# Kernel tuning notes

Hardware: AMD Instinct MI355X
Metric: run time of the kernel (lower is better)

## Reference

```python
import jax, jax.numpy as jnp
import numpy as np

NUM_HEADS = 8
GROUPS = 32
EPS = 1e-5


def group_norm(x, gamma, beta):
    # x: [b, c, l]; normalize over (c//GROUPS, l) per group
    b, c, l = x.shape
    xg = x.reshape(b, GROUPS, -1)
    mu = jnp.mean(xg, axis=-1, keepdims=True)
    var = jnp.mean(jnp.square(xg - mu), axis=-1, keepdims=True)
    xn = ((xg - mu) * jax.lax.rsqrt(var + EPS)).reshape(b, c, l)
    return xn * gamma[None, :, None] + beta[None, :, None]


def setup_inputs() -> dict:
    key = jax.random.key(0)
    ks = jax.random.split(key, 8)
    b, c, h, w = 8, 512, 64, 64
    cc, cl = 768, 256
    inner = 512
    s = lambda fan_in: 1.0 / np.sqrt(fan_in)
    return {
        "x": jax.random.normal(ks[0], (b, c, h, w), jnp.float32),
        "context": jax.random.normal(ks[1], (b, cc, cl), jnp.float32),
        "gnx_g": jnp.ones((c,), jnp.float32),
        "gnx_b": jnp.zeros((c,), jnp.float32),
        "gnc_g": jnp.ones((cc,), jnp.float32),
        "gnc_b": jnp.zeros((cc,), jnp.float32),
        "wq": jax.random.normal(ks[2], (inner, c), jnp.float32) * s(c),
        "bq": jax.random.normal(ks[3], (inner,), jnp.float32) * s(c),
        "wkv": jax.random.normal(ks[4], (2 * inner, cc), jnp.float32) * s(cc),
        "bkv": jax.random.normal(ks[5], (2 * inner,), jnp.float32) * s(cc),
        "wo": jax.random.normal(ks[6], (c, inner), jnp.float32) * s(inner),
        "bo": jax.random.normal(ks[7], (c,), jnp.float32) * s(inner),
    }


def reference(x, context, gnx_g, gnx_b, gnc_g, gnc_b, wq, bq, wkv, bkv, wo, bo):
    b, c, h, w = x.shape
    xf = x.reshape(b, c, h * w)                      # [b, c, L]
    inner = wq.shape[0]
    dh = inner // NUM_HEADS
    scale = dh ** (-0.5)

    q = jnp.einsum('oc,bcl->bol', wq, group_norm(xf, gnx_g, gnx_b)) + bq[None, :, None]
    kv = jnp.einsum('oc,bcl->bol', wkv, group_norm(context, gnc_g, gnc_b)) + bkv[None, :, None]
    k, v = jnp.split(kv, 2, axis=1)                  # [b, inner, S] each

    L = xf.shape[-1]
    S = k.shape[-1]
    q = q.reshape(b * NUM_HEADS, dh, L)
    k = k.reshape(b * NUM_HEADS, dh, S)
    v = v.reshape(b * NUM_HEADS, dh, S)

    # Faithful double-scale quirk: effective scaling is 1/dh
    dots = jnp.einsum('bct,bcs->bts', q * scale, k * scale)   # [bH, L, S]
    attn = jax.nn.softmax(dots.astype(jnp.float32), axis=-1).astype(dots.dtype)
    out = jnp.einsum('bts,bcs->bct', attn, v)                 # [bH, dh, L]
    out = out.reshape(b, inner, L)
    out = jnp.einsum('oc,bcl->bol', wo, out) + bo[None, :, None]
    return (xf + out).reshape(b, c, h, w)
```

## Files before the change

kernel.cpp:

```cpp
#include <hip/hip_runtime.h>

typedef unsigned short u16;
typedef unsigned int u32;
typedef __bf16 bf16x8 __attribute__((ext_vector_type(8)));
typedef float f32x4 __attribute__((ext_vector_type(4)));

__device__ __forceinline__ u16 f2bf(float f) {
    return __builtin_bit_cast(u16, (__bf16)f);
}
__device__ __forceinline__ u32 pkbf(float a, float b) {
    return (u32)__builtin_bit_cast(u16, (__bf16)a) |
           ((u32)__builtin_bit_cast(u16, (__bf16)b) << 16);
}
__device__ __forceinline__ u32 pku(u16 a, u16 b) {
    return (u32)a | ((u32)b << 16);
}
__device__ __forceinline__ bf16x8 ldb8(const void* p) {
    return __builtin_bit_cast(bf16x8, *(const uint4*)p);
}
__device__ __forceinline__ f32x4 mfma16(bf16x8 a, bf16x8 b, f32x4 c) {
    return __builtin_amdgcn_mfma_f32_16x16x32_bf16(a, b, c, 0, 0, 0);
}

__global__ __launch_bounds__(256) void cvt_w(const float* __restrict__ in,
                                             u16* __restrict__ out, int n4) {
    int i = blockIdx.x * 256 + threadIdx.x;
    const int stride = gridDim.x * 256;
    for (; i < n4; i += stride) {
        float4 v = ((const float4*)in)[i];
        ((uint2*)out)[i] = make_uint2(pkbf(v.x, v.y), pkbf(v.z, v.w));
    }
}

__global__ __launch_bounds__(256) void gn_stats(const float* __restrict__ in,
                                                float2* __restrict__ stats, int N) {
    const int tid = threadIdx.x;
    const long base = (long)blockIdx.x * N;
    float s = 0.f, s2 = 0.f;
    for (int i = tid * 4; i < N; i += 256 * 4) {
        float4 v = *(const float4*)(in + base + i);
        s += v.x + v.y + v.z + v.w;
        s2 += v.x * v.x + v.y * v.y + v.z * v.z + v.w * v.w;
    }
#pragma unroll
    for (int m = 1; m < 64; m <<= 1) { s += __shfl_xor(s, m); s2 += __shfl_xor(s2, m); }
    __shared__ float ps[4], ps2[4];
    const int w = tid >> 6;
    if ((tid & 63) == 0) { ps[w] = s; ps2[w] = s2; }
    __syncthreads();
    if (tid == 0) {
        float S = ps[0] + ps[1] + ps[2] + ps[3];
        float S2 = ps2[0] + ps2[1] + ps2[2] + ps2[3];
        float mu = S / (float)N;
        float var = S2 / (float)N - mu * mu;
        stats[blockIdx.x] = make_float2(mu, rsqrtf(var + 1e-5f));
    }
}


__global__ __launch_bounds__(256) void gn_tr(const float* __restrict__ ctx,
                                             const float2* __restrict__ stats,
                                             const float* __restrict__ gamma,
                                             const float* __restrict__ beta,
                                             u16* __restrict__ ctx_t) {
    __shared__ u16 T[64][64];
    const int tid = threadIdx.x;
    const int b = blockIdx.z;
    const int c0 = blockIdx.x * 64, s0 = blockIdx.y * 64;
#pragma unroll
    for (int r = 0; r < 4; ++r) {
        int idx = r * 256 + tid;
        int c = idx >> 4, s4 = (idx & 15) << 2;
        int cg = c0 + c;
        float4 v = *(const float4*)(ctx + ((long)b * 768 + cg) * 256 + s0 + s4);
        float2 st = stats[b * 32 + cg / 24];
        float gm = gamma[cg], bt = beta[cg];
        float vv[4] = {(v.x - st.x) * st.y * gm + bt, (v.y - st.x) * st.y * gm + bt,
                       (v.z - st.x) * st.y * gm + bt, (v.w - st.x) * st.y * gm + bt};
#pragma unroll
        for (int jj = 0; jj < 4; ++jj) {
            int j = (jj + (tid & 3)) & 3;
            int row = s4 + j;
            T[row][c ^ ((row & 7) << 3)] = f2bf(vv[j]);
        }
    }
    __syncthreads();
#pragma unroll
    for (int r = 0; r < 2; ++r) {
        int f = r * 256 + tid;
        int s = f >> 3, cf = (f & 7) << 3;
        uint4 vv = *(const uint4*)&T[s][cf ^ ((s & 7) << 3)];
        *(uint4*)(ctx_t + ((long)b * 256 + s0 + s) * 768 + c0 + cf) = vv;
    }
}

__global__ __launch_bounds__(256, 2) void gemm_kv2(
    const u16* __restrict__ W, const u16* __restrict__ ctx_t,
    const float* __restrict__ bias, u16* __restrict__ k_t, u16* __restrict__ vout) {
    constexpr int K = 768;
    const int tid = threadIdx.x;
    const int b = blockIdx.z;
    const int o0 = blockIdx.x * 64;
    const int s0 = blockIdx.y * 64;
    const int lane = tid & 63, wv = tid >> 6;
    const int l16 = lane & 15, g = lane >> 4;

    const u16* ap = W + (long)(o0 + wv * 16 + l16) * K;
    const u16* ct = ctx_t + ((long)b * 256 + s0) * K;

    f32x4 acc[4] = {};
#pragma unroll
    for (int kc = 0; kc < 24; ++kc) {
        const int k8 = kc * 32 + g * 8;
        bf16x8 afr = ldb8(ap + k8);
#pragma unroll
        for (int ni = 0; ni < 4; ++ni) {
            bf16x8 bfr = ldb8(ct + (long)(ni * 16 + l16) * K + k8);
            acc[ni] = mfma16(afr, bfr, acc[ni]);
        }
    }
    const int orow = o0 + wv * 16 + g * 4;
    if (blockIdx.x < 8) {
        const int h = blockIdx.x;
        const int d0 = wv * 16 + g * 4;
        const float b0 = bias[orow], b1 = bias[orow + 1];
        const float b2 = bias[orow + 2], b3 = bias[orow + 3];
#pragma unroll
        for (int ni = 0; ni < 4; ++ni) {
            int s = s0 + ni * 16 + l16;
            *(uint2*)(k_t + (((long)b * 8 + h) * 256 + s) * 64 + d0) =
                make_uint2(pkbf(acc[ni][0] + b0, acc[ni][1] + b1),
                           pkbf(acc[ni][2] + b2, acc[ni][3] + b3));
        }
    } else {
#pragma unroll
        for (int ni = 0; ni < 4; ++ni) {
            int s = s0 + ni * 16 + l16;
#pragma unroll
            for (int i = 0; i < 4; ++i) {
                int vr = orow - 512 + i;
                vout[((long)b * 512 + vr) * 256 + s] = f2bf(acc[ni][i] + bias[orow + i]);
            }
        }
    }
}

template <int MODE>
__global__ __launch_bounds__(256, 2) void big_gemm(
    const u16* __restrict__ W, const void* __restrict__ Bsrc,
    const float2* __restrict__ stats, const float* __restrict__ gamma,
    const float* __restrict__ beta, const float* __restrict__ bias,
    const float* __restrict__ X, void* __restrict__ outp) {
    constexpr int K = 512, N = 4096, CPG = 16;
    __shared__ u16 Blds[64][64];
    const int tid = threadIdx.x;
    const int b = blockIdx.z;
    const int n0 = blockIdx.x * 64;
    const int lane = tid & 63, w = tid >> 6;
    const int l16 = lane & 15, g = lane >> 4;

    f32x4 acc[8][4] = {};
    for (int c = 0; c < 8; ++c) {
        const int k0 = c * 64;
        __syncthreads();
        if (MODE == 0) {
            const float* Bb = (const float*)Bsrc + (long)b * K * N;
#pragma unroll
            for (int r = 0; r < 4; ++r) {
                int idx = r * 256 + tid;
                int kk = idx >> 4;
                int n4 = (idx & 15) << 2;
                int kg = k0 + kk;
                float4 v = *(const float4*)(Bb + (long)kg * N + n0 + n4);
                float2 st = stats[b * 32 + kg / CPG];
                float gm = gamma[kg], bt = beta[kg];
                v.x = (v.x - st.x) * st.y * gm + bt;
                v.y = (v.y - st.x) * st.y * gm + bt;
                v.z = (v.z - st.x) * st.y * gm + bt;
                v.w = (v.w - st.x) * st.y * gm + bt;
                float vv[4] = {v.x, v.y, v.z, v.w};
#pragma unroll
                for (int jj = 0; jj < 4; ++jj) {
                    int j = (jj + (lane & 3)) & 3;
                    int row = n4 + j;
                    Blds[row][kk ^ ((row & 7) << 3)] = f2bf(vv[j]);
                }
            }
        } else {
            const u16* Ob = (const u16*)Bsrc + (((long)b * 8 + c) * 4096 + n0) * 64;
#pragma unroll
            for (int r = 0; r < 2; ++r) {
                int idx = r * 256 + tid;
                int t = idx >> 3;
                int d0 = (idx & 7) << 3;
                uint4 vv = *(const uint4*)(Ob + (long)t * 64 + d0);
                *(uint4*)&Blds[t][d0 ^ ((t & 7) << 3)] = vv;
            }
        }
        __syncthreads();
#pragma unroll
        for (int kk = 0; kk < 2; ++kk) {
            bf16x8 bfr[4];
#pragma unroll
            for (int ni = 0; ni < 4; ++ni) {
                int row = ni * 16 + l16;
                bfr[ni] = ldb8(&Blds[row][(kk * 32 + g * 8) ^ ((row & 7) << 3)]);
            }
#pragma unroll
            for (int mi = 0; mi < 8; ++mi) {
                int arow = w * 128 + mi * 16 + l16;
                bf16x8 afr = ldb8(W + (long)arow * K + k0 + kk * 32 + g * 8);
#pragma unroll
                for (int ni = 0; ni < 4; ++ni)
                    acc[mi][ni] = mfma16(afr, bfr[ni], acc[mi][ni]);
            }
        }
    }
    if (MODE == 0) {
        u16* qt = (u16*)outp;
#pragma unroll
        for (int mi = 0; mi < 8; ++mi) {
            int h = w * 2 + (mi >> 2);
            int dbase = (mi & 3) * 16 + g * 4;
#pragma unroll
            for (int ni = 0; ni < 4; ++ni) {
                int col = n0 + ni * 16 + l16;
                float v0 = acc[mi][ni][0] + bias[h * 64 + dbase + 0];
                float v1 = acc[mi][ni][1] + bias[h * 64 + dbase + 1];
                float v2 = acc[mi][ni][2] + bias[h * 64 + dbase + 2];
                float v3 = acc[mi][ni][3] + bias[h * 64 + dbase + 3];
                *(uint2*)(qt + (((long)b * 8 + h) * 4096 + col) * 64 + dbase) =
                    make_uint2(pkbf(v0, v1), pkbf(v2, v3));
            }
        }
    } else {
        float* out = (float*)outp;
        const long ob = (long)b * K * N;
#pragma unroll
        for (int mi = 0; mi < 8; ++mi)
#pragma unroll
            for (int i = 0; i < 4; ++i) {
                int row = w * 128 + mi * 16 + g * 4 + i;
                float bs = bias[row];
#pragma unroll
                for (int ni = 0; ni < 4; ++ni) {
                    int col = n0 + ni * 16 + l16;
                    long off = ob + (long)row * N + col;
                    out[off] = acc[mi][ni][i] + bs + X[off];
                }
            }
    }
}

__global__ __launch_bounds__(256, 1) void attn_v9(const u16* __restrict__ qt_in,
                                                  const u16* __restrict__ k_t,
                                                  const u16* __restrict__ v,
                                                  u16* __restrict__ qt_out) {
    __shared__ u16 kT[256][64];
    __shared__ u16 Vp[64][256];
    const int tid = threadIdx.x;
    const int bh = blockIdx.y;
    const int b = bh >> 3, h = bh & 7;
    const int lane = tid & 63, w = tid >> 6;
    const int l16 = lane & 15, g = lane >> 4;

    const long kb = (long)bh * 256 * 64;
    const long vb = ((long)(b * 512 + h * 64)) * 256;
    const long qb = (long)bh * 4096 * 64 + (long)blockIdx.x * 512 * 64;

#pragma unroll
    for (int r = 0; r < 8; ++r) {
        int idx = r * 256 + tid;
        int s = idx >> 3, d0 = (idx & 7) << 3;
        uint4 vv = *(const uint4*)(k_t + kb + (long)s * 64 + d0);
        *(uint4*)&kT[s][d0 ^ ((s & 7) << 3)] = vv;
    }
#pragma unroll
    for (int r = 0; r < 8; ++r) {
        int idx = r * 256 + tid;
        int d = idx >> 5, s0 = (idx & 31) << 3;
        union { uint4 v4; u16 h8[8]; } u;
        u.v4 = *(const uint4*)(v + vb + (long)d * 256 + s0);
        int f = s0 >> 4, g2 = (s0 >> 2) & 3;
        int cl = ((f >> 1) << 5) + (g2 << 3) + ((f & 1) << 2);
        int sw = (d & 7) << 3;
        *(uint2*)&Vp[d][cl ^ sw] = make_uint2(pku(u.h8[0], u.h8[1]), pku(u.h8[2], u.h8[3]));
        *(uint2*)&Vp[d][(cl + 8) ^ sw] = make_uint2(pku(u.h8[4], u.h8[5]), pku(u.h8[6], u.h8[7]));
    }
    __syncthreads();

    const float aa = 0.015625f * 1.44269504f;
    bf16x8 bq0, bq1;
    {
        const u16* qp = qt_in + qb + (long)(w * 16 + l16) * 64;
        bq0 = ldb8(qp + g * 8);
        bq1 = ldb8(qp + 32 + g * 8);
    }
    for (int it = 0; it < 8; ++it) {
        const int tcol = it * 64 + w * 16 + l16;
        f32x4 sacc[16] = {};
#pragma unroll
        for (int mc = 0; mc < 4; ++mc) {
#pragma unroll
            for (int kk = 0; kk < 2; ++kk) {
                bf16x8 bqk = kk ? bq1 : bq0;
#pragma unroll
                for (int j = 0; j < 4; ++j) {
                    int mi = mc * 4 + j;
                    bf16x8 ak = ldb8(&kT[mi * 16 + l16][(kk * 32 + g * 8) ^ ((l16 & 7) << 3)]);
                    sacc[mi] = mfma16(ak, bqk, sacc[mi]);
                }
            }
        }
        if (it < 7) {
            const u16* qp = qt_in + qb + (long)(tcol + 64) * 64;
            bq0 = ldb8(qp + g * 8);
            bq1 = ldb8(qp + 32 + g * 8);
        }
        float s0 = 0.f, s1 = 0.f, s2 = 0.f, s3 = 0.f;
#pragma unroll
        for (int f = 0; f < 16; ++f) {
            float p0 = exp2f(sacc[f][0] * aa);
            float p1 = exp2f(sacc[f][1] * aa);
            float p2 = exp2f(sacc[f][2] * aa);
            float p3 = exp2f(sacc[f][3] * aa);
            sacc[f][0] = p0; sacc[f][1] = p1; sacc[f][2] = p2; sacc[f][3] = p3;
            s0 += p0; s1 += p1; s2 += p2; s3 += p3;
        }
        float sum = (s0 + s1) + (s2 + s3);
        sum += __shfl_xor(sum, 16);
        sum += __shfl_xor(sum, 32);
        const float inv = 1.0f / sum;
        f32x4 oacc[4] = {};
#pragma unroll
        for (int ks = 0; ks < 8; ++ks) {
            bf16x8 bp = __builtin_bit_cast(bf16x8,
                make_uint4(pkbf(sacc[2 * ks][0], sacc[2 * ks][1]),
                           pkbf(sacc[2 * ks][2], sacc[2 * ks][3]),
                           pkbf(sacc[2 * ks + 1][0], sacc[2 * ks + 1][1]),
                           pkbf(sacc[2 * ks + 1][2], sacc[2 * ks + 1][3])));
#pragma unroll
            for (int mi = 0; mi < 4; ++mi) {
                bf16x8 av = ldb8(&Vp[mi * 16 + l16][(ks * 32 + g * 8) ^ ((l16 & 7) << 3)]);
                oacc[mi] = mfma16(av, bp, oacc[mi]);
            }
        }
        u16* op = qt_out + qb + (long)tcol * 64;
#pragma unroll
        for (int mi = 0; mi < 4; ++mi) {
            *(uint2*)(op + mi * 16 + g * 4) = make_uint2(
                pkbf(oacc[mi][0] * inv, oacc[mi][1] * inv),
                pkbf(oacc[mi][2] * inv, oacc[mi][3] * inv));
        }
    }
}

template <bool GN, bool RESID>
__global__ __launch_bounds__(256, 2) void big_gemm_f32(
    const u16* __restrict__ W, const float* __restrict__ B,
    const float2* __restrict__ stats, const float* __restrict__ gamma,
    const float* __restrict__ beta, const float* __restrict__ bias,
    const float* __restrict__ X, float* __restrict__ out) {
    constexpr int K = 512, N = 4096, CPG = 16;
    __shared__ u16 Blds[64][64];
    const int tid = threadIdx.x;
    const int b = blockIdx.z;
    const int n0 = blockIdx.x * 64;
    const int lane = tid & 63, w = tid >> 6;
    const int l16 = lane & 15, g = lane >> 4;
    const float* Bb = B + (long)b * K * N;

    f32x4 acc[8][4] = {};
    for (int c = 0; c < 8; ++c) {
        const int k0 = c * 64;
        __syncthreads();
#pragma unroll
        for (int r = 0; r < 4; ++r) {
            int idx = r * 256 + tid;
            int kk = idx >> 4;
            int n4 = (idx & 15) << 2;
            int kg = k0 + kk;
            float4 v = *(const float4*)(Bb + (long)kg * N + n0 + n4);
            if (GN) {
                float2 st = stats[b * 32 + kg / CPG];
                float gm = gamma[kg], bt = beta[kg];
                v.x = (v.x - st.x) * st.y * gm + bt;
                v.y = (v.y - st.x) * st.y * gm + bt;
                v.z = (v.z - st.x) * st.y * gm + bt;
                v.w = (v.w - st.x) * st.y * gm + bt;
            }
            float vv[4] = {v.x, v.y, v.z, v.w};
#pragma unroll
            for (int jj = 0; jj < 4; ++jj) {
                int j = (jj + (lane & 3)) & 3;
                int row = n4 + j;
                Blds[row][kk ^ ((row & 7) << 3)] = f2bf(vv[j]);
            }
        }
        __syncthreads();
#pragma unroll
        for (int kk = 0; kk < 2; ++kk) {
            bf16x8 bfr[4];
#pragma unroll
            for (int ni = 0; ni < 4; ++ni) {
                int row = ni * 16 + l16;
                bfr[ni] = ldb8(&Blds[row][(kk * 32 + g * 8) ^ ((row & 7) << 3)]);
            }
#pragma unroll
            for (int mi = 0; mi < 8; ++mi) {
                int arow = w * 128 + mi * 16 + l16;
                bf16x8 afr = ldb8(W + (long)arow * K + k0 + kk * 32 + g * 8);
#pragma unroll
                for (int ni = 0; ni < 4; ++ni)
                    acc[mi][ni] = mfma16(afr, bfr[ni], acc[mi][ni]);
            }
        }
    }
    const long ob = (long)b * K * N;
#pragma unroll
    for (int mi = 0; mi < 8; ++mi)
#pragma unroll
        for (int i = 0; i < 4; ++i) {
            int row = w * 128 + mi * 16 + g * 4 + i;
            float bs = bias[row];
#pragma unroll
            for (int ni = 0; ni < 4; ++ni) {
                int col = n0 + ni * 16 + l16;
                long off = ob + (long)row * N + col;
                float v = acc[mi][ni][i] + bs;
                if (RESID) v += X[off];
                out[off] = v;
            }
        }
}

__global__ __launch_bounds__(256) void gemm_kv_old(
    const u16* __restrict__ W, const float* __restrict__ act,
    const float2* __restrict__ stats, const float* __restrict__ gamma,
    const float* __restrict__ beta, const float* __restrict__ bias,
    u16* __restrict__ outp, int K, int N, int CPG, long actBS, long outBS) {
    __shared__ u16 Blds[128][40];
    const int tid = threadIdx.x;
    const int b = blockIdx.z;
    const int m0 = blockIdx.y * 128;
    const int n0 = blockIdx.x * 128;
    const int lane = tid & 63;
    const int w = tid >> 6;
    const int wr = w >> 1, wc = w & 1;
    const int l16 = lane & 15, g = lane >> 4;

    const float* actB = act + (long)b * actBS;
    f32x4 acc[4][4] = {};
    for (int s = 0; s < K / 32; ++s) {
        const int k0 = s * 32;
        __syncthreads();
#pragma unroll
        for (int r = 0; r < 4; ++r) {
            int idx = r * 256 + tid;
            int kk = idx >> 5;
            int n4 = (idx & 31) << 2;
            int kg = k0 + kk;
            float2 st = stats[b * 32 + kg / CPG];
            float gm = gamma[kg], bt = beta[kg];
            float4 v = *(const float4*)(actB + (long)kg * N + n0 + n4);
            Blds[n4 + 0][kk] = f2bf((v.x - st.x) * st.y * gm + bt);
            Blds[n4 + 1][kk] = f2bf((v.y - st.x) * st.y * gm + bt);
            Blds[n4 + 2][kk] = f2bf((v.z - st.x) * st.y * gm + bt);
            Blds[n4 + 3][kk] = f2bf((v.w - st.x) * st.y * gm + bt);
        }
        __syncthreads();
        bf16x8 bfr[4];
#pragma unroll
        for (int ni = 0; ni < 4; ++ni)
            bfr[ni] = ldb8(&Blds[wc * 64 + ni * 16 + l16][g * 8]);
#pragma unroll
        for (int mi = 0; mi < 4; ++mi) {
            int row = m0 + wr * 64 + mi * 16 + l16;
            bf16x8 afr = ldb8(W + (long)row * K + k0 + g * 8);
#pragma unroll
            for (int ni = 0; ni < 4; ++ni)
                acc[mi][ni] = mfma16(afr, bfr[ni], acc[mi][ni]);
        }
    }
#pragma unroll
    for (int mi = 0; mi < 4; ++mi)
#pragma unroll
        for (int i = 0; i < 4; ++i) {
            int row = m0 + wr * 64 + mi * 16 + g * 4 + i;
            float bs = bias[row];
#pragma unroll
            for (int ni = 0; ni < 4; ++ni) {
                int col = n0 + wc * 64 + ni * 16 + l16;
                outp[(long)b * outBS + (long)row * N + col] = f2bf(acc[mi][ni][i] + bs);
            }
        }
}

__global__ __launch_bounds__(256, 2) void attn_v4(const float* q,
                                                  const u16* __restrict__ kv,
                                                  float* out) {
    __shared__ u16 kT[256][64];
    __shared__ u16 Vp[64][256];
    const int tid = threadIdx.x;
    const int bh = blockIdx.y;
    const int b = bh >> 3, h = bh & 7;
    const int lane = tid & 63, w = tid >> 6;
    const int l16 = lane & 15, g = lane >> 4;

    const long kbase = ((long)(b * 1024 + h * 64)) * 256;
    const long vbase = ((long)(b * 1024 + 512 + h * 64)) * 256;
    const long qb = ((long)(b * 512 + h * 64)) * 4096 + blockIdx.x * 512;

#pragma unroll
    for (int r = 0; r < 8; ++r) {
        int idx = r * 256 + tid;
        int d = idx >> 5, s8 = idx & 31;
        union { uint4 v; u16 h8[8]; } u;
        u.v = *(const uint4*)(kv + kbase + (long)d * 256 + s8 * 8);
#pragma unroll
        for (int j = 0; j < 8; ++j)
            kT[s8 * 8 + j][d ^ (j << 3)] = u.h8[j];
    }
#pragma unroll
    for (int r = 0; r < 8; ++r) {
        int idx = r * 256 + tid;
        int d = idx >> 5, s0 = (idx & 31) << 3;
        union { uint4 v; u16 h8[8]; } u;
        u.v = *(const uint4*)(kv + vbase + (long)d * 256 + s0);
        int f = s0 >> 4, g2 = (s0 >> 2) & 3;
        int cl = ((f >> 1) << 5) + (g2 << 3) + ((f & 1) << 2);
        int sw = (d & 7) << 3;
        *(uint2*)&Vp[d][cl ^ sw] = make_uint2(pku(u.h8[0], u.h8[1]), pku(u.h8[2], u.h8[3]));
        *(uint2*)&Vp[d][(cl + 8) ^ sw] = make_uint2(pku(u.h8[4], u.h8[5]), pku(u.h8[6], u.h8[7]));
    }
    __syncthreads();

    const float aa = 0.015625f * 1.44269504f;
    for (int it = 0; it < 8; ++it) {
        const int tcol = it * 64 + w * 16 + l16;
        u32 bqw[2][4];
#pragma unroll
        for (int kk = 0; kk < 2; ++kk) {
            const float* qp = q + qb + tcol + (long)(kk * 32 + g * 8) * 4096;
#pragma unroll
            for (int jp = 0; jp < 4; ++jp)
                bqw[kk][jp] = pkbf(qp[(2 * jp) * 4096], qp[(2 * jp + 1) * 4096]);
        }
        f32x4 sacc[16] = {};
#pragma unroll
        for (int kk = 0; kk < 2; ++kk) {
            bf16x8 bq_ = __builtin_bit_cast(bf16x8,
                make_uint4(bqw[kk][0], bqw[kk][1], bqw[kk][2], bqw[kk][3]));
#pragma unroll
            for (int mi = 0; mi < 16; ++mi) {
                bf16x8 ak = ldb8(&kT[mi * 16 + l16][(kk * 32 + g * 8) ^ ((l16 & 7) << 3)]);
                sacc[mi] = mfma16(ak, bq_, sacc[mi]);
            }
        }
        float m = -3e38f;
#pragma unroll
        for (int f = 0; f < 16; ++f)
#pragma unroll
            for (int i = 0; i < 4; ++i) m = fmaxf(m, sacc[f][i]);
        m = fmaxf(m, __shfl_xor(m, 16));
        m = fmaxf(m, __shfl_xor(m, 32));
        float m2 = m * aa;
        float sum = 0.f;
#pragma unroll
        for (int f = 0; f < 16; ++f)
#pragma unroll
            for (int i = 0; i < 4; ++i) {
                float p = exp2f(fmaf(sacc[f][i], aa, -m2));
                sacc[f][i] = p;
                sum += p;
            }
        sum += __shfl_xor(sum, 16);
        sum += __shfl_xor(sum, 32);
        const float inv = 1.0f / sum;
        f32x4 oacc[4] = {};
#pragma unroll
        for (int ks = 0; ks < 8; ++ks) {
            bf16x8 bp = __builtin_bit_cast(bf16x8,
                make_uint4(pkbf(sacc[2 * ks][0], sacc[2 * ks][1]),
                           pkbf(sacc[2 * ks][2], sacc[2 * ks][3]),
                           pkbf(sacc[2 * ks + 1][0], sacc[2 * ks + 1][1]),
                           pkbf(sacc[2 * ks + 1][2], sacc[2 * ks + 1][3])));
#pragma unroll
            for (int mi = 0; mi < 4; ++mi) {
                bf16x8 av = ldb8(&Vp[mi * 16 + l16][(ks * 32 + g * 8) ^ ((l16 & 7) << 3)]);
                oacc[mi] = mfma16(av, bp, oacc[mi]);
            }
        }
#pragma unroll
        for (int mi = 0; mi < 4; ++mi)
#pragma unroll
            for (int i = 0; i < 4; ++i)
                out[qb + (long)(mi * 16 + g * 4 + i) * 4096 + tcol] = oacc[mi][i] * inv;
    }
}

extern "C" void kernel_launch(void* const* d_in, const int* in_sizes, int n_in,
                              void* d_out, int out_size, void* d_ws, size_t ws_size,
                              hipStream_t stream) {
    const float* x     = (const float*)d_in[0];
    const float* ctx   = (const float*)d_in[1];
    const float* gnx_g = (const float*)d_in[2];
    const float* gnx_b = (const float*)d_in[3];
    const float* gnc_g = (const float*)d_in[4];
    const float* gnc_b = (const float*)d_in[5];
    const float* wq    = (const float*)d_in[6];
    const float* bq    = (const float*)d_in[7];
    const float* wkv   = (const float*)d_in[8];
    const float* bkv   = (const float*)d_in[9];
    const float* wo    = (const float*)d_in[10];
    const float* bo    = (const float*)d_in[11];
    float* out = (float*)d_out;

    char* ws = (char*)d_ws;
    float2* stats_x = (float2*)ws;
    float2* stats_c = (float2*)(ws + 2048);
    u16* wq_bf  = (u16*)(ws + 4096);
    u16* wkv_bf = (u16*)(ws + 528384);
    u16* wo_bf  = (u16*)(ws + 2101248);

    cvt_w<<<dim3(256), dim3(256), 0, stream>>>(wq, wq_bf, 512 * 512 / 4);
    cvt_w<<<dim3(256), dim3(256), 0, stream>>>(wkv, wkv_bf, 1024 * 768 / 4);
    cvt_w<<<dim3(256), dim3(256), 0, stream>>>(wo, wo_bf, 512 * 512 / 4);
    gn_stats<<<dim3(256), dim3(256), 0, stream>>>(x, stats_x, 16 * 4096);
    gn_stats<<<dim3(256), dim3(256), 0, stream>>>(ctx, stats_c, 24 * 256);

    const size_t NEED = 40374272;
    if (ws_size >= NEED) {
        u16* k_t   = (u16*)(ws + 2625536);
        u16* v     = (u16*)(ws + 4722688);
        u16* q_t   = (u16*)(ws + 6819840);
        u16* ctx_t = (u16*)(ws + 6819840);

        gn_tr<<<dim3(12, 4, 8), dim3(256), 0, stream>>>(
            ctx, stats_c, gnc_g, gnc_b, ctx_t);
        gemm_kv2<<<dim3(16, 4, 8), dim3(256), 0, stream>>>(
            wkv_bf, ctx_t, bkv, k_t, v);
        big_gemm<0><<<dim3(64, 1, 8), dim3(256), 0, stream>>>(
            wq_bf, x, stats_x, gnx_g, gnx_b, bq, nullptr, q_t);
        attn_v9<<<dim3(8, 64), dim3(256), 0, stream>>>(q_t, k_t, v, q_t);
        big_gemm<1><<<dim3(64, 1, 8), dim3(256), 0, stream>>>(
            wo_bf, q_t, nullptr, nullptr, nullptr, bo, x, out);
    } else {
        u16* kv = (u16*)(ws + 2625536);
        big_gemm_f32<true, false><<<dim3(64, 1, 8), dim3(256), 0, stream>>>(
            wq_bf, x, stats_x, gnx_g, gnx_b, bq, nullptr, out);
        gemm_kv_old<<<dim3(2, 8, 8), dim3(256), 0, stream>>>(
            wkv_bf, ctx, stats_c, gnc_g, gnc_b, bkv, kv, 768, 256, 24,
            (long)768 * 256, (long)1024 * 256);
        attn_v4<<<dim3(8, 64), dim3(256), 0, stream>>>(out, kv, out);
        big_gemm_f32<false, true><<<dim3(64, 1, 8), dim3(256), 0, stream>>>(
            wo_bf, out, nullptr, nullptr, nullptr, bo, x, out);
    }
}
```

Baseline: 232.2 us.

## Split attention S tile into halves to cut registers and allow two blocks per CU

The attention kernel now computes scores, exponentials and the PV product in two halves of 128 keys each, packing probabilities to bf16 right away, so only 8 score accumulators are live at a time instead of 16. Launch bounds are raised to two blocks per CU so the lower register pressure can turn into higher occupancy. The Q prefetch for the next iteration is dropped, and each iteration loads its Q fragment directly. The trade-off is less latency hiding inside a wave in exchange for more waves per CU. LDS usage (64 KB per block) may also cap occupancy.

```diff
diff --git a/kernel.cpp b/kernel.cpp
--- a/kernel.cpp
+++ b/kernel.cpp
@@ -252,10 +252,10 @@
     }
 }
 
-__global__ __launch_bounds__(256, 1) void attn_v9(const u16* __restrict__ qt_in,
-                                                  const u16* __restrict__ k_t,
-                                                  const u16* __restrict__ v,
-                                                  u16* __restrict__ qt_out) {
+__global__ __launch_bounds__(256, 2) void attn_v10(const u16* __restrict__ qt_in,
+                                                   const u16* __restrict__ k_t,
+                                                   const u16* __restrict__ v,
+                                                   u16* __restrict__ qt_out) {
     __shared__ u16 kT[256][64];
     __shared__ u16 Vp[64][256];
     const int tid = threadIdx.x;
@@ -290,61 +290,61 @@
     __syncthreads();
 
     const float aa = 0.015625f * 1.44269504f;
-    bf16x8 bq0, bq1;
-    {
-        const u16* qp = qt_in + qb + (long)(w * 16 + l16) * 64;
-        bq0 = ldb8(qp + g * 8);
-        bq1 = ldb8(qp + 32 + g * 8);
-    }
     for (int it = 0; it < 8; ++it) {
         const int tcol = it * 64 + w * 16 + l16;
-        f32x4 sacc[16] = {};
-#pragma unroll
-        for (int mc = 0; mc < 4; ++mc) {
-#pragma unroll
-            for (int kk = 0; kk < 2; ++kk) {
-                bf16x8 bqk = kk ? bq1 : bq0;
-#pragma unroll
-                for (int j = 0; j < 4; ++j) {
-                    int mi = mc * 4 + j;
-                    bf16x8 ak = ldb8(&kT[mi * 16 + l16][(kk * 32 + g * 8) ^ ((l16 & 7) << 3)]);
-                    sacc[mi] = mfma16(ak, bqk, sacc[mi]);
+        const u16* qp = qt_in + qb + (long)tcol * 64;
+        bf16x8 bq0 = ldb8(qp + g * 8);
+        bf16x8 bq1 = ldb8(qp + 32 + g * 8);
+
+        f32x4 oacc[4] = {};
+        float sum = 0.f;
+#pragma unroll
+        for (int half = 0; half < 2; ++half) {
+            f32x4 sacc[8] = {};
+#pragma unroll
+            for (int mc = 0; mc < 2; ++mc) {
+#pragma unroll
+                for (int kk = 0; kk < 2; ++kk) {
+                    bf16x8 bqk = kk ? bq1 : bq0;
+#pragma unroll
+                    for (int j = 0; j < 4; ++j) {
+                        int fl = mc * 4 + j;
+                        int mi = half * 8 + fl;
+                        bf16x8 ak =
+                            ldb8(&kT[mi * 16 + l16][(kk * 32 + g * 8) ^ ((l16 & 7) << 3)]);
+                        sacc[fl] = mfma16(ak, bqk, sacc[fl]);
+                    }
                 }
             }
-        }
-        if (it < 7) {
-            const u16* qp = qt_in + qb + (long)(tcol + 64) * 64;
-            bq0 = ldb8(qp + g * 8);
-            bq1 = ldb8(qp + 32 + g * 8);
-        }
-        float s0 = 0.f, s1 = 0.f, s2 = 0.f, s3 = 0.f;
-#pragma unroll
-        for (int f = 0; f < 16; ++f) {
-            float p0 = exp2f(sacc[f][0] * aa);
-            float p1 = exp2f(sacc[f][1] * aa);
-            float p2 = exp2f(sacc[f][2] * aa);
-            float p3 = exp2f(sacc[f][3] * aa);
-            sacc[f][0] = p0; sacc[f][1] = p1; sacc[f][2] = p2; sacc[f][3] = p3;
-            s0 += p0; s1 += p1; s2 += p2; s3 += p3;
-        }
-        float sum = (s0 + s1) + (s2 + s3);
+            u32 pk[8][2];
+            float s0 = 0.f, s1 = 0.f, s2 = 0.f, s3 = 0.f;
+#pragma unroll
+            for (int f = 0; f < 8; ++f) {
+                float p0 = exp2f(sacc[f][0] * aa);
+                float p1 = exp2f(sacc[f][1] * aa);
+                float p2 = exp2f(sacc[f][2] * aa);
+                float p3 = exp2f(sacc[f][3] * aa);
+                pk[f][0] = pkbf(p0, p1);
+                pk[f][1] = pkbf(p2, p3);
+                s0 += p0; s1 += p1; s2 += p2; s3 += p3;
+            }
+            sum += (s0 + s1) + (s2 + s3);
+#pragma unroll
+            for (int ks2 = 0; ks2 < 4; ++ks2) {
+                int ks = half * 4 + ks2;
+                bf16x8 bp = __builtin_bit_cast(bf16x8,
+                    make_uint4(pk[2 * ks2][0], pk[2 * ks2][1],
+                               pk[2 * ks2 + 1][0], pk[2 * ks2 + 1][1]));
+#pragma unroll
+                for (int mi = 0; mi < 4; ++mi) {
+                    bf16x8 av = ldb8(&Vp[mi * 16 + l16][(ks * 32 + g * 8) ^ ((l16 & 7) << 3)]);
+                    oacc[mi] = mfma16(av, bp, oacc[mi]);
+                }
+            }
+        }
         sum += __shfl_xor(sum, 16);
         sum += __shfl_xor(sum, 32);
         const float inv = 1.0f / sum;
-        f32x4 oacc[4] = {};
-#pragma unroll
-        for (int ks = 0; ks < 8; ++ks) {
-            bf16x8 bp = __builtin_bit_cast(bf16x8,
-                make_uint4(pkbf(sacc[2 * ks][0], sacc[2 * ks][1]),
-                           pkbf(sacc[2 * ks][2], sacc[2 * ks][3]),
-                           pkbf(sacc[2 * ks + 1][0], sacc[2 * ks + 1][1]),
-                           pkbf(sacc[2 * ks + 1][2], sacc[2 * ks + 1][3])));
-#pragma unroll
-            for (int mi = 0; mi < 4; ++mi) {
-                bf16x8 av = ldb8(&Vp[mi * 16 + l16][(ks * 32 + g * 8) ^ ((l16 & 7) << 3)]);
-                oacc[mi] = mfma16(av, bp, oacc[mi]);
-            }
-        }
         u16* op = qt_out + qb + (long)tcol * 64;
 #pragma unroll
         for (int mi = 0; mi < 4; ++mi) {
@@ -642,7 +642,7 @@
             wkv_bf, ctx_t, bkv, k_t, v);
         big_gemm<0><<<dim3(64, 1, 8), dim3(256), 0, stream>>>(
             wq_bf, x, stats_x, gnx_g, gnx_b, bq, nullptr, q_t);
-        attn_v9<<<dim3(8, 64), dim3(256), 0, stream>>>(q_t, k_t, v, q_t);
+        attn_v10<<<dim3(8, 64), dim3(256), 0, stream>>>(q_t, k_t, v, q_t);
         big_gemm<1><<<dim3(64, 1, 8), dim3(256), 0, stream>>>(
             wo_bf, q_t, nullptr, nullptr, nullptr, bo, x, out);
     } else {
```

Measured after the change: 288.9 us. +24.4%, slower.

## Double attention block to 512 threads and add max-subtracted softmax

Applied to the files above, without the earlier changes.

The attention kernel now launches with 512 threads (8 waves) per block. The cooperative K/V shared-memory staging is split across more threads, and each block runs 4 query-tile iterations instead of 8. The software prefetch of the next Q fragment is dropped in favour of loading Q at the top of each iteration. Softmax now subtracts a per-row max before exp2 for numerical safety, which adds a max-reduction pass and cross-lane shuffles.

```diff
diff --git a/kernel.cpp b/kernel.cpp
--- a/kernel.cpp
+++ b/kernel.cpp
@@ -252,10 +252,10 @@
     }
 }
 
-__global__ __launch_bounds__(256, 1) void attn_v9(const u16* __restrict__ qt_in,
-                                                  const u16* __restrict__ k_t,
-                                                  const u16* __restrict__ v,
-                                                  u16* __restrict__ qt_out) {
+__global__ __launch_bounds__(512, 1) void attn_v11(const u16* __restrict__ qt_in,
+                                                   const u16* __restrict__ k_t,
+                                                   const u16* __restrict__ v,
+                                                   u16* __restrict__ qt_out) {
     __shared__ u16 kT[256][64];
     __shared__ u16 Vp[64][256];
     const int tid = threadIdx.x;
@@ -269,15 +269,15 @@
     const long qb = (long)bh * 4096 * 64 + (long)blockIdx.x * 512 * 64;
 
 #pragma unroll
-    for (int r = 0; r < 8; ++r) {
-        int idx = r * 256 + tid;
+    for (int r = 0; r < 4; ++r) {
+        int idx = r * 512 + tid;
         int s = idx >> 3, d0 = (idx & 7) << 3;
         uint4 vv = *(const uint4*)(k_t + kb + (long)s * 64 + d0);
         *(uint4*)&kT[s][d0 ^ ((s & 7) << 3)] = vv;
     }
 #pragma unroll
-    for (int r = 0; r < 8; ++r) {
-        int idx = r * 256 + tid;
+    for (int r = 0; r < 4; ++r) {
+        int idx = r * 512 + tid;
         int d = idx >> 5, s0 = (idx & 31) << 3;
         union { uint4 v4; u16 h8[8]; } u;
         u.v4 = *(const uint4*)(v + vb + (long)d * 256 + s0);
@@ -290,14 +290,11 @@
     __syncthreads();
 
     const float aa = 0.015625f * 1.44269504f;
-    bf16x8 bq0, bq1;
-    {
-        const u16* qp = qt_in + qb + (long)(w * 16 + l16) * 64;
-        bq0 = ldb8(qp + g * 8);
-        bq1 = ldb8(qp + 32 + g * 8);
-    }
-    for (int it = 0; it < 8; ++it) {
-        const int tcol = it * 64 + w * 16 + l16;
+    for (int it = 0; it < 4; ++it) {
+        const int tcol = it * 128 + w * 16 + l16;
+        const u16* qp = qt_in + qb + (long)tcol * 64;
+        bf16x8 bq0 = ldb8(qp + g * 8);
+        bf16x8 bq1 = ldb8(qp + 32 + g * 8);
         f32x4 sacc[16] = {};
 #pragma unroll
         for (int mc = 0; mc < 4; ++mc) {
@@ -312,22 +309,23 @@
                 }
             }
         }
-        if (it < 7) {
-            const u16* qp = qt_in + qb + (long)(tcol + 64) * 64;
-            bq0 = ldb8(qp + g * 8);
-            bq1 = ldb8(qp + 32 + g * 8);
-        }
-        float s0 = 0.f, s1 = 0.f, s2 = 0.f, s3 = 0.f;
-#pragma unroll
-        for (int f = 0; f < 16; ++f) {
-            float p0 = exp2f(sacc[f][0] * aa);
-            float p1 = exp2f(sacc[f][1] * aa);
-            float p2 = exp2f(sacc[f][2] * aa);
-            float p3 = exp2f(sacc[f][3] * aa);
-            sacc[f][0] = p0; sacc[f][1] = p1; sacc[f][2] = p2; sacc[f][3] = p3;
-            s0 += p0; s1 += p1; s2 += p2; s3 += p3;
-        }
-        float sum = (s0 + s1) + (s2 + s3);
+        float m = -3e38f;
+#pragma unroll
+        for (int f = 0; f < 16; ++f)
+#pragma unroll
+            for (int i = 0; i < 4; ++i) m = fmaxf(m, sacc[f][i]);
+        m = fmaxf(m, __shfl_xor(m, 16));
+        m = fmaxf(m, __shfl_xor(m, 32));
+        float m2 = m * aa;
+        float sum = 0.f;
+#pragma unroll
+        for (int f = 0; f < 16; ++f)
+#pragma unroll
+            for (int i = 0; i < 4; ++i) {
+                float p = exp2f(fmaf(sacc[f][i], aa, -m2));
+                sacc[f][i] = p;
+                sum += p;
+            }
         sum += __shfl_xor(sum, 16);
         sum += __shfl_xor(sum, 32);
         const float inv = 1.0f / sum;
@@ -642,7 +640,7 @@
             wkv_bf, ctx_t, bkv, k_t, v);
         big_gemm<0><<<dim3(64, 1, 8), dim3(256), 0, stream>>>(
             wq_bf, x, stats_x, gnx_g, gnx_b, bq, nullptr, q_t);
-        attn_v9<<<dim3(8, 64), dim3(256), 0, stream>>>(q_t, k_t, v, q_t);
+        attn_v11<<<dim3(8, 64), dim3(512), 0, stream>>>(q_t, k_t, v, q_t);
         big_gemm<1><<<dim3(64, 1, 8), dim3(256), 0, stream>>>(
             wo_bf, q_t, nullptr, nullptr, nullptr, bo, x, out);
     } else {
```

Measured after the change: 267.5 us. +15.2%, slower.
